# Kernel optimization log

Measured on AMD Instinct MI355X. Metric: run time of the kernel, lower is better.

## Reference

```python
import jax, jax.numpy as jnp
import numpy as np

# --- static mask-construction config (mirrors FlexAttnFunc.init_mask args) ---
B = 1
L_F, L_H, L_W = 8, 20, 36      # latent_shape[2:]
A_F, A_H, A_W = 8, 1, 1        # action_shape[2:]
PATCH = (1, 2, 2)
CHUNK = 1
PAD = 176
WINDOW = 6
DIM, HEADS, DHEAD = 1536, 12, 128
EPS = 1e-5


def _make_ids():
    lf, lh, lw = L_F // PATCH[0], L_H // PATCH[1], L_W // PATCH[2]
    lat_seq = np.repeat(np.arange(B), lf * lh * lw)
    act_seq = np.repeat(np.arange(B), A_F * A_H * A_W)
    seq = np.concatenate([lat_seq, lat_seq, act_seq, act_seq])
    lat_fr = np.broadcast_to(np.arange(L_F)[None, :, None, None], (B, L_F, lh, lw)).reshape(-1)
    act_fr = np.broadcast_to(np.arange(A_F)[None, :, None, None], (B, A_F, A_H, A_W)).reshape(-1)
    fr = np.concatenate([lat_fr // CHUNK * 2] * 2 + [act_fr // CHUNK * 2 + 1] * 2)
    nz = np.concatenate([np.zeros_like(lat_fr), np.ones_like(lat_fr),
                         np.zeros_like(act_fr), np.ones_like(act_fr)])
    pad = np.full(PAD, -1, dtype=np.int64)
    return (np.concatenate([seq, pad]).astype(np.int32),
            np.concatenate([fr, pad]).astype(np.int32),
            np.concatenate([nz, pad]).astype(np.int32))


def setup_inputs() -> dict:
    key = jax.random.key(0)
    ks = jax.random.split(key, 8)
    seq, fr, nz = _make_ids()
    S = seq.shape[0]  # 3072
    sd = 0.02
    return {
        'x': jax.random.normal(ks[0], (1, S, DIM), jnp.float32),
        'Wq': jax.random.normal(ks[1], (DIM, DIM), jnp.float32) * sd,
        'bq': jnp.zeros((DIM,), jnp.float32),
        'Wk': jax.random.normal(ks[2], (DIM, DIM), jnp.float32) * sd,
        'bk': jnp.zeros((DIM,), jnp.float32),
        'Wv': jax.random.normal(ks[3], (DIM, DIM), jnp.float32) * sd,
        'bv': jnp.zeros((DIM,), jnp.float32),
        'gq': 1.0 + jax.random.normal(ks[4], (DIM,), jnp.float32) * sd,
        'gk': 1.0 + jax.random.normal(ks[5], (DIM,), jnp.float32) * sd,
        'Wo': jax.random.normal(ks[6], (DIM, DIM), jnp.float32) * sd,
        'bo': jnp.zeros((DIM,), jnp.float32),
        'seq_ids': jnp.asarray(seq),
        'frame_ids': jnp.asarray(fr),
        'noise_ids': jnp.asarray(nz),
        'window_size': WINDOW,
    }


def _rms(u, g):
    # torch.nn.RMSNorm over last dim (size heads*dim_head), elementwise affine
    return u * jax.lax.rsqrt(jnp.mean(u * u, axis=-1, keepdims=True) + EPS) * g


def _mask(seq_ids, frame_ids, noise_ids, window_size):
    sq, sk = seq_ids[:, None], seq_ids[None, :]
    fq, fk = frame_ids[:, None], frame_ids[None, :]
    nq, nk = noise_ids[:, None], noise_ids[None, :]
    seq_ok = (sq == sk) & (sq >= 0) & (sk >= 0)
    c2c = (nq == 1) & (nk == 1) & (fk <= fq)      # clean->clean, block causal incl self
    n2c = (nq == 0) & (nk == 1) & (fk < fq)       # noise->clean, causal excl self
    n2n = (nq == 0) & (nk == 0) & (fk == fq)      # noise->noise, same frame only
    win = jnp.abs(fq - fk) <= window_size
    return (c2c | n2c | n2n) & seq_ok & win


def reference(x, Wq, bq, Wk, bk, Wv, bv, gq, gk, Wo, bo,
              seq_ids, frame_ids, noise_ids, window_size):
    S = x.shape[1]
    q = _rms(x @ Wq + bq, gq)[0].reshape(S, HEADS, DHEAD)
    k = _rms(x @ Wk + bk, gk)[0].reshape(S, HEADS, DHEAD)
    v = (x @ Wv + bv)[0].reshape(S, HEADS, DHEAD)
    mask = _mask(seq_ids, frame_ids, noise_ids, window_size)  # [S,S] bool
    scores = jnp.einsum('qhd,khd->hqk', q, k) * (DHEAD ** -0.5)
    scores = jnp.where(mask[None], scores, jnp.float32(-1e9))
    attn = jax.nn.softmax(scores, axis=-1)
    o = jnp.einsum('hqk,khd->qhd', attn, v)
    # zero out padded (fully-masked) query rows
    o = o * (seq_ids >= 0).astype(o.dtype)[:, None, None]
    y = o.reshape(1, S, HEADS * DHEAD) @ Wo + bo
    return y
```

## Files before the change

### kernel.cpp

```cpp
#include <hip/hip_runtime.h>
#include <hip/hip_bf16.h>
#include <stdint.h>

typedef __bf16 bf16x8 __attribute__((ext_vector_type(8)));
typedef float f32x4 __attribute__((ext_vector_type(4)));

__device__ __forceinline__ unsigned short f2bf(float f) {
  union { float f; unsigned int u; } v; v.f = f;
  unsigned int u = v.u;
  unsigned int r = (u + 0x7fffu + ((u >> 16) & 1u)) >> 16;
  return (unsigned short)r;
}

__global__ __launch_bounds__(256) void conv_f2bf(const float* __restrict__ in,
                                                 unsigned short* __restrict__ out, int n4) {
  int i = blockIdx.x * 256 + threadIdx.x;
  if (i < n4) {
    float4 v = ((const float4*)in)[i];
    ushort4 o;
    o.x = f2bf(v.x); o.y = f2bf(v.y); o.z = f2bf(v.z); o.w = f2bf(v.w);
    ((ushort4*)out)[i] = o;
  }
}

__global__ __launch_bounds__(256) void prep_bitmap(const int* __restrict__ seq,
                                                   const int* __restrict__ fr,
                                                   const int* __restrict__ nz,
                                                   const int* __restrict__ wsz,
                                                   unsigned long long* __restrict__ tbm,
                                                   int S) {
  __shared__ int ks_[3072];
  __shared__ unsigned int tm_[96];
  int tid = threadIdx.x, W = wsz[0];
  for (int i = tid; i < S; i += 256) {
    int sq = seq[i];
    ks_[i] = (sq < 0) ? 0 : ((1 << 9) | ((nz[i] & 1) << 8) | (fr[i] & 15) | (sq << 10));
  }
  __syncthreads();
  for (int t = tid; t < S / 32; t += 256) {
    unsigned int m = 0;
    for (int j = 0; j < 32; j++) {
      int a = ks_[t * 32 + j];
      if (a & (1 << 9)) m |= (a & (1 << 8)) ? (1u << (16 + (a & 15))) : (1u << (a & 15));
    }
    tm_[t] = m;
  }
  __syncthreads();
  for (int qg = tid; qg < S / 16; qg += 256) {
    unsigned int allowed = 0;
    for (int j = 0; j < 16; j++) {
      int a = ks_[qg * 16 + j];
      if (!(a & (1 << 9))) continue;
      int fq = a & 15, nq = (a >> 8) & 1;
      int lo = fq - W; if (lo < 0) lo = 0;
      unsigned int lom = ~((1u << lo) - 1);
      if (nq) allowed |= (((1u << (fq + 1)) - 1) & lom) << 16;
      else    allowed |= ((((1u << fq) - 1) & lom) << 16) | (1u << fq);
    }
    unsigned long long b0 = 0, b1 = 0;
    for (int t = 0; t < 96; t++)
      if (tm_[t] & allowed) { if (t < 64) b0 |= 1ull << t; else b1 |= 1ull << (t - 64); }
    tbm[qg * 2] = b0; tbm[qg * 2 + 1] = b1;
  }
}

__global__ __launch_bounds__(256) void prep_mask(const int* __restrict__ seq,
                                                 const int* __restrict__ fr,
                                                 const int* __restrict__ nz,
                                                 const int* __restrict__ wsz,
                                                 unsigned char* __restrict__ mb, int S) {
  int qg = blockIdx.y, t0 = blockIdx.x * 4;
  __shared__ int qs[16], qf_[16], qn[16], ksq[128], kfr[128], knz[128];
  int tid = threadIdx.x;
  if (tid < 16) {
    int q = qg * 16 + tid; qs[tid] = seq[q]; qf_[tid] = fr[q]; qn[tid] = nz[q];
  } else if (tid < 144) {
    int i = tid - 16; int k = t0 * 32 + i;
    ksq[i] = seq[k]; kfr[i] = fr[k]; knz[i] = nz[k];
  }
  __syncthreads();
  int wave = tid >> 6, lane = tid & 63, quad = lane >> 4, l16 = lane & 15;
  int W = wsz[0];
  unsigned int byte = 0;
  for (int nt = 0; nt < 2; nt++)
    for (int r = 0; r < 4; r++) {
      int qi = quad * 4 + r;
      int ki = wave * 32 + nt * 16 + l16;
      bool ok  = (qs[qi] == ksq[ki]) && (qs[qi] >= 0) && (ksq[ki] >= 0);
      bool c2c = (qn[qi] == 1) && (knz[ki] == 1) && (kfr[ki] <= qf_[qi]);
      bool n2c = (qn[qi] == 0) && (knz[ki] == 1) && (kfr[ki] <  qf_[qi]);
      bool n2n = (qn[qi] == 0) && (knz[ki] == 0) && (kfr[ki] == qf_[qi]);
      int df = qf_[qi] - kfr[ki]; df = df < 0 ? -df : df;
      if ((c2c || n2c || n2n) && ok && (df <= W)) byte |= 1u << (nt * 4 + r);
    }
  mb[((size_t)qg * 96 + t0 + wave) * 64 + lane] = (unsigned char)byte;
}

__global__ __launch_bounds__(256) void conv_wt4(const float* __restrict__ W0,
                                                const float* __restrict__ W1,
                                                const float* __restrict__ W2,
                                                const float* __restrict__ W3,
                                                unsigned short* __restrict__ Wt) {
  const int K = 1536, N = 1536;
  const float* W = blockIdx.z == 0 ? W0 : (blockIdx.z == 1 ? W1 : (blockIdx.z == 2 ? W2 : W3));
  __shared__ __align__(16) unsigned short t[64][65];
  int k0 = blockIdx.x * 64, n0 = blockIdx.y * 64;
  for (int i = 0; i < 16; i++) {
    int e = threadIdx.x + i * 256;
    int r = e >> 6, c = e & 63;
    t[r][c] = f2bf(W[(size_t)(k0 + r) * N + n0 + c]);
  }
  __syncthreads();
  for (int i = 0; i < 16; i++) {
    int e = threadIdx.x + i * 256;
    int r = e >> 6, c = e & 63;
    Wt[(size_t)(blockIdx.z * 1536 + n0 + r) * K + k0 + c] = t[c][r];
  }
}

__global__ __launch_bounds__(256) void gemm_qkv(
    const unsigned short* __restrict__ A, const unsigned short* __restrict__ Bt,
    const float* __restrict__ bq, const float* __restrict__ bk, const float* __restrict__ bv,
    float* __restrict__ linq, float* __restrict__ link, unsigned short* __restrict__ vtb,
    int S) {
  const int K = 1536;
  __shared__ __align__(16) unsigned short As[128 * 64];
  __shared__ __align__(16) unsigned short Bs[128 * 64];
  int tid = threadIdx.x, wave = tid >> 6, lane = tid & 63;
  int quad = lane >> 4, l16 = lane & 15;
  int m0 = blockIdx.x * 128, n0 = blockIdx.y * 128;
  int wm = (wave & 1) * 64, wn = (wave >> 1) * 64;
  int lr = lane >> 3, lc = (lane & 7) * 8;
  f32x4 acc[4][4] = {};
  for (int k0 = 0; k0 < K; k0 += 64) {
    for (int c = 0; c < 4; c++) {
      int chunk = wave * 4 + c;
      int row = chunk * 8 + lr;
      const unsigned short* ga = &A[(size_t)(m0 + row) * K + k0 + lc];
      const unsigned short* gb = &Bt[(size_t)(n0 + row) * K + k0 + lc];
      __builtin_amdgcn_global_load_lds(
          (const __attribute__((address_space(1))) unsigned int*)ga,
          (__attribute__((address_space(3))) unsigned int*)(As + chunk * 512), 16, 0, 0);
      __builtin_amdgcn_global_load_lds(
          (const __attribute__((address_space(1))) unsigned int*)gb,
          (__attribute__((address_space(3))) unsigned int*)(Bs + chunk * 512), 16, 0, 0);
    }
    __syncthreads();
    for (int kk = 0; kk < 64; kk += 32) {
      bf16x8 af[4], bfr[4];
      for (int i = 0; i < 4; i++)
        af[i] = *(const bf16x8*)&As[(wm + i * 16 + l16) * 64 + kk + quad * 8];
      for (int j = 0; j < 4; j++)
        bfr[j] = *(const bf16x8*)&Bs[(wn + j * 16 + l16) * 64 + kk + quad * 8];
      for (int i = 0; i < 4; i++)
        for (int j = 0; j < 4; j++)
          acc[i][j] = __builtin_amdgcn_mfma_f32_16x16x32_bf16(af[i], bfr[j], acc[i][j], 0, 0, 0);
    }
    __syncthreads();
  }
  int region = (n0 >= 3072) ? 2 : (n0 >= 1536 ? 1 : 0);
  int cbase = n0 - region * 1536;
  if (region < 2) {
    float* lin = region == 0 ? linq : link;
    const float* bias = region == 0 ? bq : bk;
    for (int j = 0; j < 4; j++) {
      int col = cbase + wn + j * 16 + l16;
      float b = bias[col];
      for (int i = 0; i < 4; i++)
        for (int r = 0; r < 4; r++)
          lin[(size_t)(m0 + wm + i * 16 + quad * 4 + r) * 1536 + col] = acc[i][j][r] + b;
    }
  } else {
    for (int j = 0; j < 4; j++) {
      int d = cbase + wn + j * 16 + l16;
      float b = bv[d];
      int hh = d >> 7, dd = d & 127;
      for (int i = 0; i < 4; i++)
        for (int r = 0; r < 4; r++) {
          int s = m0 + wm + i * 16 + quad * 4 + r;
          vtb[((size_t)(hh * 96 + (s >> 5)) * 128 + dd) * 32 + (s & 31)] = f2bf(acc[i][j][r] + b);
        }
    }
  }
}

__global__ __launch_bounds__(256) void gemm_wo(
    const unsigned short* __restrict__ A, const unsigned short* __restrict__ Bt,
    const float* __restrict__ bias, float* __restrict__ C, int M, int N, int K) {
  __shared__ __align__(16) unsigned short As[128 * 64];
  __shared__ __align__(16) unsigned short Bs[64 * 64];
  int tid = threadIdx.x, wave = tid >> 6, lane = tid & 63;
  int quad = lane >> 4, l16 = lane & 15;
  int m0 = blockIdx.x * 128, n0 = blockIdx.y * 64;
  int wm = (wave & 1) * 64, wn = (wave >> 1) * 32;
  int lr = lane >> 3, lc = (lane & 7) * 8;
  f32x4 acc[4][2] = {};
  for (int k0 = 0; k0 < K; k0 += 64) {
    for (int c = 0; c < 4; c++) {
      int chunk = wave * 4 + c;
      int row = chunk * 8 + lr;
      const unsigned short* ga = &A[(size_t)(m0 + row) * K + k0 + lc];
      __builtin_amdgcn_global_load_lds(
          (const __attribute__((address_space(1))) unsigned int*)ga,
          (__attribute__((address_space(3))) unsigned int*)(As + chunk * 512), 16, 0, 0);
    }
    for (int c = 0; c < 2; c++) {
      int chunk = wave * 2 + c;
      int row = chunk * 8 + lr;
      const unsigned short* gb = &Bt[(size_t)(n0 + row) * K + k0 + lc];
      __builtin_amdgcn_global_load_lds(
          (const __attribute__((address_space(1))) unsigned int*)gb,
          (__attribute__((address_space(3))) unsigned int*)(Bs + chunk * 512), 16, 0, 0);
    }
    __syncthreads();
    for (int kk = 0; kk < 64; kk += 32) {
      bf16x8 af[4], bfr[2];
      for (int i = 0; i < 4; i++)
        af[i] = *(const bf16x8*)&As[(wm + i * 16 + l16) * 64 + kk + quad * 8];
      for (int j = 0; j < 2; j++)
        bfr[j] = *(const bf16x8*)&Bs[(wn + j * 16 + l16) * 64 + kk + quad * 8];
      for (int i = 0; i < 4; i++)
        for (int j = 0; j < 2; j++)
          acc[i][j] = __builtin_amdgcn_mfma_f32_16x16x32_bf16(af[i], bfr[j], acc[i][j], 0, 0, 0);
    }
    __syncthreads();
  }
  for (int j = 0; j < 2; j++) {
    int col = n0 + wn + j * 16 + l16;
    float b = bias[col];
    for (int i = 0; i < 4; i++)
      for (int r = 0; r < 4; r++)
        C[(size_t)(m0 + wm + i * 16 + quad * 4 + r) * N + col] = acc[i][j][r] + b;
  }
}

__global__ __launch_bounds__(256) void rms_bf16(const float* __restrict__ lin,
                                                const float* __restrict__ g,
                                                unsigned short* __restrict__ out,
                                                int mode) {
  const int N = 1536;
  int row = blockIdx.x;
  const float* p = lin + (size_t)row * N;
  float vals[6];
  float ss = 0.f;
  for (int j = 0; j < 6; j++) {
    float v = p[threadIdx.x + j * 256];
    vals[j] = v; ss += v * v;
  }
  for (int o = 32; o > 0; o >>= 1) ss += __shfl_down(ss, o);
  __shared__ float red[4];
  if ((threadIdx.x & 63) == 0) red[threadIdx.x >> 6] = ss;
  __syncthreads();
  float tot = red[0] + red[1] + red[2] + red[3];
  float sc = rsqrtf(tot * (1.0f / N) + 1e-5f);
  for (int j = 0; j < 6; j++) {
    int c = threadIdx.x + j * 256;
    int hh = c >> 7, dd = c & 127;
    unsigned short v = f2bf(vals[j] * sc * g[c]);
    if (mode == 1)
      out[(((size_t)(hh * 96 + (row >> 5)) * 32) + (row & 31)) * 128 + dd] = v;
    else
      out[(((size_t)(hh * 192 + (row >> 4)) * 16) + (row & 15)) * 128 + dd] = v;
  }
}

__global__ __launch_bounds__(256) void attn(
    const unsigned short* __restrict__ qt,
    const unsigned short* __restrict__ kt,
    const unsigned short* __restrict__ vt,
    const unsigned char* __restrict__ mb,
    const unsigned long long* __restrict__ tbm,
    float* __restrict__ op0, float* __restrict__ op1,
    float* __restrict__ lp, int S) {
  const int h = blockIdx.x;
  const int qb64 = blockIdx.y;
  const int split = blockIdx.z;
  int tid = threadIdx.x, wave = tid >> 6, lane = tid & 63;
  int quad = lane >> 4, l16 = lane & 15;
  const float scale = 0.088388347648318447f;

  __shared__ __align__(16) unsigned short Ks[2][4096];
  __shared__ __align__(16) unsigned short Vs[2][4096];
  __shared__ __align__(16) unsigned short pshare[4][16][40];

  int qg = qb64 * 4 + wave;
  unsigned long long bm0 = tbm[(qb64 * 4) * 2]     | tbm[(qb64 * 4 + 1) * 2] |
                           tbm[(qb64 * 4 + 2) * 2] | tbm[(qb64 * 4 + 3) * 2];
  unsigned long long bm1 = tbm[(qb64 * 4) * 2 + 1]     | tbm[(qb64 * 4 + 1) * 2 + 1] |
                           tbm[(qb64 * 4 + 2) * 2 + 1] | tbm[(qb64 * 4 + 3) * 2 + 1];
  unsigned long long wb0 = tbm[qg * 2], wb1 = tbm[qg * 2 + 1];

  const unsigned short* kth = kt + (size_t)h * 96 * 4096;
  const unsigned short* vth = vt + (size_t)h * 96 * 4096;
  const unsigned char* mbq = mb + (size_t)qg * 96 * 64;

  bf16x8 qf[4];
  {
    const unsigned short* qp = qt + ((size_t)(h * 192 + qg) * 16 + l16) * 128 + quad * 8;
    for (int ks = 0; ks < 4; ks++) qf[ks] = *(const bf16x8*)&qp[ks * 32];
  }

  f32x4 oacc[8] = {};
  f32x4 lacc = {};
  const __bf16 onebf = (__bf16)1.0f;
  const bf16x8 ones = {onebf, onebf, onebf, onebf, onebf, onebf, onebf, onebf};

#define POP(dst) do { \
    if (bm0) { dst = __builtin_ctzll(bm0); bm0 &= bm0 - 1; } \
    else if (bm1) { dst = 64 + __builtin_ctzll(bm1); bm1 &= bm1 - 1; } \
    else dst = -1; } while (0)

#define STAGE(t_, b_) do { \
    for (int j = 0; j < 2; j++) { \
      int slot = j * 256 + tid; \
      int key = slot >> 4, cc = slot & 15; \
      const unsigned short* src = kth + (size_t)(t_) * 4096 + key * 128 + (cc ^ (key & 15)) * 8; \
      __builtin_amdgcn_global_load_lds( \
          (const __attribute__((address_space(1))) unsigned int*)src, \
          (__attribute__((address_space(3))) unsigned int*)(&Ks[b_][0] + j * 2048 + wave * 512), \
          16, 0, 0); \
    } \
    for (int j = 0; j < 2; j++) { \
      int slot = j * 256 + tid; \
      int row = slot >> 2, cc = slot & 3; \
      const unsigned short* src = vth + (size_t)(t_) * 4096 + row * 32 + (cc ^ ((row >> 1) & 3)) * 8; \
      __builtin_amdgcn_global_load_lds( \
          (const __attribute__((address_space(1))) unsigned int*)src, \
          (__attribute__((address_space(3))) unsigned int*)(&Vs[b_][0] + j * 2048 + wave * 512), \
          16, 0, 0); \
    } } while (0)

  int t, dsc;
  if (split) POP(dsc);
  POP(t);
  unsigned int mbyte = 0;
  if (t >= 0) { STAGE(t, 0); mbyte = mbq[t * 64 + lane]; }
  __syncthreads();
  int buf = 0;

  while (t >= 0) {
    POP(dsc);
    int tn; POP(tn);
    unsigned int mbyte2 = 0;
    if (tn >= 0) { STAGE(tn, buf ^ 1); mbyte2 = mbq[tn * 64 + lane]; }

    bool live = (t < 64) ? ((wb0 >> t) & 1) : ((wb1 >> (t - 64)) & 1);
    if (live) {
      f32x4 sacc[2] = {};
      for (int nt = 0; nt < 2; nt++) {
        int key = nt * 16 + l16;
        for (int ks = 0; ks < 4; ks++) {
          int cc = (ks * 4 + quad) ^ l16;
          bf16x8 kf = *(const bf16x8*)&Ks[buf][(key * 16 + cc) * 8];
          sacc[nt] = __builtin_amdgcn_mfma_f32_16x16x32_bf16(qf[ks], kf, sacc[nt], 0, 0, 0);
        }
      }
      for (int nt = 0; nt < 2; nt++)
        for (int r = 0; r < 4; r++) {
          float e = __expf(sacc[nt][r] * scale - 16.0f);
          float p = ((mbyte >> (nt * 4 + r)) & 1) ? e : 0.0f;
          pshare[wave][quad * 4 + r][nt * 16 + l16] = f2bf(p);
        }
      __asm__ __volatile__("s_waitcnt lgkmcnt(0)" ::: "memory");
      bf16x8 pf = *(const bf16x8*)&pshare[wave][l16][quad * 8];
      for (int d = 0; d < 8; d++) {
        int row = d * 16 + l16;
        int cc = quad ^ ((l16 >> 1) & 3);
        bf16x8 vf = *(const bf16x8*)&Vs[buf][(row * 4 + cc) * 8];
        oacc[d] = __builtin_amdgcn_mfma_f32_16x16x32_bf16(pf, vf, oacc[d], 0, 0, 0);
      }
      lacc = __builtin_amdgcn_mfma_f32_16x16x32_bf16(pf, ones, lacc, 0, 0, 0);
    }
    __syncthreads();
    buf ^= 1;
    t = tn;
    mbyte = mbyte2;
  }
#undef POP
#undef STAGE

  float* po = split ? op1 : op0;
  for (int r = 0; r < 4; r++) {
    int q = qb64 * 64 + wave * 16 + quad * 4 + r;
    for (int d = 0; d < 8; d++)
      po[((size_t)h * S + q) * 128 + d * 16 + l16] = oacc[d][r];
    if (l16 == 0)
      lp[((size_t)split * 12 + h) * S + q] = lacc[r];
  }
}

__global__ __launch_bounds__(256) void combine(const float* __restrict__ op0,
                                               const float* __restrict__ op1,
                                               const float* __restrict__ lp,
                                               const int* __restrict__ seq,
                                               unsigned short* __restrict__ ob, int S) {
  int e4 = blockIdx.x * 256 + threadIdx.x;
  int idx = e4 * 4;
  int per_h = S * 128;
  int h = idx / per_h;
  int rem = idx - h * per_h;
  int q = rem >> 7, dd = rem & 127;
  float l = lp[(size_t)h * S + q] + lp[(size_t)(12 + h) * S + q];
  float inv = (seq[q] >= 0 && l > 0.f) ? 1.0f / l : 0.0f;
  float4 a = ((const float4*)op0)[e4];
  float4 b = ((const float4*)op1)[e4];
  ushort4 o;
  o.x = f2bf((a.x + b.x) * inv);
  o.y = f2bf((a.y + b.y) * inv);
  o.z = f2bf((a.z + b.z) * inv);
  o.w = f2bf((a.w + b.w) * inv);
  *(ushort4*)&ob[(size_t)q * 1536 + h * 128 + dd] = o;
}

extern "C" void kernel_launch(void* const* d_in, const int* in_sizes, int n_in,
                              void* d_out, int out_size, void* d_ws, size_t ws_size,
                              hipStream_t stream) {
  const float* x  = (const float*)d_in[0];
  const float* Wq = (const float*)d_in[1];
  const float* bq = (const float*)d_in[2];
  const float* Wk = (const float*)d_in[3];
  const float* bk = (const float*)d_in[4];
  const float* Wv = (const float*)d_in[5];
  const float* bv = (const float*)d_in[6];
  const float* gq = (const float*)d_in[7];
  const float* gk = (const float*)d_in[8];
  const float* Wo = (const float*)d_in[9];
  const float* bo = (const float*)d_in[10];
  const int* seq  = (const int*)d_in[11];
  const int* fr   = (const int*)d_in[12];
  const int* nz   = (const int*)d_in[13];
  const int* wsz  = (const int*)d_in[14];
  float* out = (float*)d_out;
  const int S = in_sizes[11];
  const int D = 1536;

  char* ws = (char*)d_ws;
  size_t off = 0;
  unsigned short* x_bf = (unsigned short*)(ws + off); off += (size_t)S * D * 2;
  unsigned short* wt   = (unsigned short*)(ws + off); off += (size_t)4 * D * D * 2;
  float*          linq = (float*)(ws + off);          off += (size_t)S * D * 4;
  float*          link = (float*)(ws + off);          off += (size_t)S * D * 4;
  unsigned short* qt   = (unsigned short*)(ws + off); off += (size_t)S * D * 2;
  unsigned short* kt   = (unsigned short*)(ws + off); off += (size_t)S * D * 2;
  unsigned short* vtb  = (unsigned short*)(ws + off); off += (size_t)S * D * 2;
  unsigned short* o_bf = (unsigned short*)(ws + off); off += (size_t)S * D * 2;
  unsigned long long* tbm = (unsigned long long*)(ws + off); off += (size_t)(S / 16) * 16;
  unsigned char*  mbuf = (unsigned char*)(ws + off);  off += (size_t)(S / 16) * 96 * 64;
  float*          lp   = (float*)(ws + off);          off += (size_t)2 * 12 * S * 4;

  dim3 blk(256);
  conv_f2bf<<<dim3((S * D / 4 + 255) / 256), blk, 0, stream>>>(x, x_bf, S * D / 4);
  prep_bitmap<<<dim3(1), blk, 0, stream>>>(seq, fr, nz, wsz, tbm, S);
  prep_mask<<<dim3(24, S / 16), blk, 0, stream>>>(seq, fr, nz, wsz, mbuf, S);
  conv_wt4<<<dim3(D / 64, D / 64, 4), blk, 0, stream>>>(Wq, Wk, Wv, Wo, wt);
  gemm_qkv<<<dim3(S / 128, 3 * D / 128), blk, 0, stream>>>(x_bf, wt, bq, bk, bv,
                                                           linq, link, vtb, S);
  rms_bf16<<<dim3(S), blk, 0, stream>>>(linq, gq, qt, 2);
  rms_bf16<<<dim3(S), blk, 0, stream>>>(link, gk, kt, 1);
  attn<<<dim3(D / 128, S / 64, 2), blk, 0, stream>>>(qt, kt, vtb, mbuf, tbm,
                                                     linq, link, lp, S);
  combine<<<dim3(12 * S * 128 / 4 / 256), blk, 0, stream>>>(linq, link, lp, seq, o_bf, S);
  gemm_wo<<<dim3(S / 128, D / 64), blk, 0, stream>>>(o_bf, wt + (size_t)3 * D * D,
                                                     bo, out, S, D, D);
}
```

Measured before the change: 329.3 us.

## Fuse RMS sum-of-squares into QKV GEMM epilogue and store bf16 partial outputs

The QKV GEMM epilogue now writes Q and K directly as bf16 in the attention layouts and accumulates per-row sums of squares into a global buffer with atomics. A small rms_scale kernel then rescales the bf16 values in place, replacing the fp32 linear intermediates and the two rms_bf16 passes. Attention split partials are normalized and stored as bf16 instead of fp32, and combine reweights them by their row sums. This is meant to cut fp32 intermediate traffic, at the cost of an extra bf16 rounding before normalization, atomic contention, and a memset launch.

```diff
diff --git a/kernel.cpp b/kernel.cpp
--- a/kernel.cpp
+++ b/kernel.cpp
@@ -10,6 +10,9 @@
   unsigned int u = v.u;
   unsigned int r = (u + 0x7fffu + ((u >> 16) & 1u)) >> 16;
   return (unsigned short)r;
+}
+__device__ __forceinline__ float bf2f(unsigned short s) {
+  union { unsigned int u; float f; } v; v.u = ((unsigned int)s) << 16; return v.f;
 }
 
 __global__ __launch_bounds__(256) void conv_f2bf(const float* __restrict__ in,
@@ -121,8 +124,8 @@
 __global__ __launch_bounds__(256) void gemm_qkv(
     const unsigned short* __restrict__ A, const unsigned short* __restrict__ Bt,
     const float* __restrict__ bq, const float* __restrict__ bk, const float* __restrict__ bv,
-    float* __restrict__ linq, float* __restrict__ link, unsigned short* __restrict__ vtb,
-    int S) {
+    unsigned short* __restrict__ qt, unsigned short* __restrict__ ktb,
+    unsigned short* __restrict__ vtb, float* __restrict__ ssq, int S) {
   const int K = 1536;
   __shared__ __align__(16) unsigned short As[128 * 64];
   __shared__ __align__(16) unsigned short Bs[128 * 64];
@@ -161,15 +164,32 @@
   int region = (n0 >= 3072) ? 2 : (n0 >= 1536 ? 1 : 0);
   int cbase = n0 - region * 1536;
   if (region < 2) {
-    float* lin = region == 0 ? linq : link;
     const float* bias = region == 0 ? bq : bk;
+    unsigned short* outp = region == 0 ? qt : ktb;
+    float* ssqp = ssq + region * 3072;
+    float ss[4][4] = {};
     for (int j = 0; j < 4; j++) {
       int col = cbase + wn + j * 16 + l16;
       float b = bias[col];
-      for (int i = 0; i < 4; i++)
-        for (int r = 0; r < 4; r++)
-          lin[(size_t)(m0 + wm + i * 16 + quad * 4 + r) * 1536 + col] = acc[i][j][r] + b;
-    }
+      int hh = col >> 7, dd = col & 127;
+      for (int i = 0; i < 4; i++)
+        for (int r = 0; r < 4; r++) {
+          float v = acc[i][j][r] + b;
+          ss[i][r] += v * v;
+          int s = m0 + wm + i * 16 + quad * 4 + r;
+          size_t idx = (region == 0)
+            ? (((size_t)(hh * 192 + (s >> 4)) * 16 + (s & 15)) * 128 + dd)
+            : (((size_t)(hh * 96  + (s >> 5)) * 32 + (s & 31)) * 128 + dd);
+          outp[idx] = f2bf(v);
+        }
+    }
+    for (int i = 0; i < 4; i++)
+      for (int r = 0; r < 4; r++) {
+        float v = ss[i][r];
+        for (int o = 1; o < 16; o <<= 1) v += __shfl_xor(v, o);
+        if (l16 == 0)
+          atomicAdd(&ssqp[m0 + wm + i * 16 + quad * 4 + r], v);
+      }
   } else {
     for (int j = 0; j < 4; j++) {
       int d = cbase + wn + j * 16 + l16;
@@ -182,6 +202,32 @@
         }
     }
   }
+}
+
+__global__ __launch_bounds__(192) void rms_scale(unsigned short* __restrict__ qt,
+                                                 unsigned short* __restrict__ ktb,
+                                                 const float* __restrict__ ssq,
+                                                 const float* __restrict__ gq,
+                                                 const float* __restrict__ gk) {
+  int row = blockIdx.x, buf = blockIdx.y;
+  unsigned short* p = buf ? ktb : qt;
+  const float* g = buf ? gk : gq;
+  float sc = rsqrtf(ssq[buf * 3072 + row] * (1.0f / 1536.0f) + 1e-5f);
+  int c = threadIdx.x * 8;
+  int hh = c >> 7, dd = c & 127;
+  size_t idx = buf
+    ? (((size_t)(hh * 96  + (row >> 5)) * 32 + (row & 31)) * 128 + dd)
+    : (((size_t)(hh * 192 + (row >> 4)) * 16 + (row & 15)) * 128 + dd);
+  ushort4 a = *(ushort4*)&p[idx];
+  ushort4 b = *(ushort4*)&p[idx + 4];
+  float4 g0 = *(const float4*)&g[c];
+  float4 g1 = *(const float4*)&g[c + 4];
+  a.x = f2bf(bf2f(a.x) * sc * g0.x); a.y = f2bf(bf2f(a.y) * sc * g0.y);
+  a.z = f2bf(bf2f(a.z) * sc * g0.z); a.w = f2bf(bf2f(a.w) * sc * g0.w);
+  b.x = f2bf(bf2f(b.x) * sc * g1.x); b.y = f2bf(bf2f(b.y) * sc * g1.y);
+  b.z = f2bf(bf2f(b.z) * sc * g1.z); b.w = f2bf(bf2f(b.w) * sc * g1.w);
+  *(ushort4*)&p[idx] = a;
+  *(ushort4*)&p[idx + 4] = b;
 }
 
 __global__ __launch_bounds__(256) void gemm_wo(
@@ -234,43 +280,13 @@
   }
 }
 
-__global__ __launch_bounds__(256) void rms_bf16(const float* __restrict__ lin,
-                                                const float* __restrict__ g,
-                                                unsigned short* __restrict__ out,
-                                                int mode) {
-  const int N = 1536;
-  int row = blockIdx.x;
-  const float* p = lin + (size_t)row * N;
-  float vals[6];
-  float ss = 0.f;
-  for (int j = 0; j < 6; j++) {
-    float v = p[threadIdx.x + j * 256];
-    vals[j] = v; ss += v * v;
-  }
-  for (int o = 32; o > 0; o >>= 1) ss += __shfl_down(ss, o);
-  __shared__ float red[4];
-  if ((threadIdx.x & 63) == 0) red[threadIdx.x >> 6] = ss;
-  __syncthreads();
-  float tot = red[0] + red[1] + red[2] + red[3];
-  float sc = rsqrtf(tot * (1.0f / N) + 1e-5f);
-  for (int j = 0; j < 6; j++) {
-    int c = threadIdx.x + j * 256;
-    int hh = c >> 7, dd = c & 127;
-    unsigned short v = f2bf(vals[j] * sc * g[c]);
-    if (mode == 1)
-      out[(((size_t)(hh * 96 + (row >> 5)) * 32) + (row & 31)) * 128 + dd] = v;
-    else
-      out[(((size_t)(hh * 192 + (row >> 4)) * 16) + (row & 15)) * 128 + dd] = v;
-  }
-}
-
 __global__ __launch_bounds__(256) void attn(
     const unsigned short* __restrict__ qt,
     const unsigned short* __restrict__ kt,
     const unsigned short* __restrict__ vt,
     const unsigned char* __restrict__ mb,
     const unsigned long long* __restrict__ tbm,
-    float* __restrict__ op0, float* __restrict__ op1,
+    unsigned short* __restrict__ op0b, unsigned short* __restrict__ op1b,
     float* __restrict__ lp, int S) {
   const int h = blockIdx.x;
   const int qb64 = blockIdx.y;
@@ -379,18 +395,19 @@
 #undef POP
 #undef STAGE
 
-  float* po = split ? op1 : op0;
+  unsigned short* po = split ? op1b : op0b;
   for (int r = 0; r < 4; r++) {
     int q = qb64 * 64 + wave * 16 + quad * 4 + r;
+    float inv = (lacc[r] > 0.f) ? 1.0f / lacc[r] : 0.0f;
     for (int d = 0; d < 8; d++)
-      po[((size_t)h * S + q) * 128 + d * 16 + l16] = oacc[d][r];
+      po[((size_t)h * S + q) * 128 + d * 16 + l16] = f2bf(oacc[d][r] * inv);
     if (l16 == 0)
       lp[((size_t)split * 12 + h) * S + q] = lacc[r];
   }
 }
 
-__global__ __launch_bounds__(256) void combine(const float* __restrict__ op0,
-                                               const float* __restrict__ op1,
+__global__ __launch_bounds__(256) void combine(const unsigned short* __restrict__ op0b,
+                                               const unsigned short* __restrict__ op1b,
                                                const float* __restrict__ lp,
                                                const int* __restrict__ seq,
                                                unsigned short* __restrict__ ob, int S) {
@@ -400,15 +417,17 @@
   int h = idx / per_h;
   int rem = idx - h * per_h;
   int q = rem >> 7, dd = rem & 127;
-  float l = lp[(size_t)h * S + q] + lp[(size_t)(12 + h) * S + q];
-  float inv = (seq[q] >= 0 && l > 0.f) ? 1.0f / l : 0.0f;
-  float4 a = ((const float4*)op0)[e4];
-  float4 b = ((const float4*)op1)[e4];
+  float l0 = lp[(size_t)h * S + q], l1 = lp[(size_t)(12 + h) * S + q];
+  float tot = l0 + l1;
+  float ok = (seq[q] >= 0 && tot > 0.f) ? 1.0f / tot : 0.0f;
+  float w0 = l0 * ok, w1 = l1 * ok;
+  ushort4 a = ((const ushort4*)op0b)[e4];
+  ushort4 b = ((const ushort4*)op1b)[e4];
   ushort4 o;
-  o.x = f2bf((a.x + b.x) * inv);
-  o.y = f2bf((a.y + b.y) * inv);
-  o.z = f2bf((a.z + b.z) * inv);
-  o.w = f2bf((a.w + b.w) * inv);
+  o.x = f2bf(bf2f(a.x) * w0 + bf2f(b.x) * w1);
+  o.y = f2bf(bf2f(a.y) * w0 + bf2f(b.y) * w1);
+  o.z = f2bf(bf2f(a.z) * w0 + bf2f(b.z) * w1);
+  o.w = f2bf(bf2f(a.w) * w0 + bf2f(b.w) * w1);
   *(ushort4*)&ob[(size_t)q * 1536 + h * 128 + dd] = o;
 }
 
@@ -438,28 +457,29 @@
   size_t off = 0;
   unsigned short* x_bf = (unsigned short*)(ws + off); off += (size_t)S * D * 2;
   unsigned short* wt   = (unsigned short*)(ws + off); off += (size_t)4 * D * D * 2;
-  float*          linq = (float*)(ws + off);          off += (size_t)S * D * 4;
-  float*          link = (float*)(ws + off);          off += (size_t)S * D * 4;
   unsigned short* qt   = (unsigned short*)(ws + off); off += (size_t)S * D * 2;
-  unsigned short* kt   = (unsigned short*)(ws + off); off += (size_t)S * D * 2;
+  unsigned short* ktb  = (unsigned short*)(ws + off); off += (size_t)S * D * 2;
   unsigned short* vtb  = (unsigned short*)(ws + off); off += (size_t)S * D * 2;
   unsigned short* o_bf = (unsigned short*)(ws + off); off += (size_t)S * D * 2;
+  unsigned short* op0b = (unsigned short*)(ws + off); off += (size_t)S * D * 2;
+  unsigned short* op1b = (unsigned short*)(ws + off); off += (size_t)S * D * 2;
   unsigned long long* tbm = (unsigned long long*)(ws + off); off += (size_t)(S / 16) * 16;
   unsigned char*  mbuf = (unsigned char*)(ws + off);  off += (size_t)(S / 16) * 96 * 64;
   float*          lp   = (float*)(ws + off);          off += (size_t)2 * 12 * S * 4;
+  float*          ssq  = (float*)(ws + off);          off += (size_t)2 * 3072 * 4;
 
   dim3 blk(256);
   conv_f2bf<<<dim3((S * D / 4 + 255) / 256), blk, 0, stream>>>(x, x_bf, S * D / 4);
   prep_bitmap<<<dim3(1), blk, 0, stream>>>(seq, fr, nz, wsz, tbm, S);
   prep_mask<<<dim3(24, S / 16), blk, 0, stream>>>(seq, fr, nz, wsz, mbuf, S);
   conv_wt4<<<dim3(D / 64, D / 64, 4), blk, 0, stream>>>(Wq, Wk, Wv, Wo, wt);
+  hipMemsetAsync(ssq, 0, (size_t)2 * 3072 * 4, stream);
   gemm_qkv<<<dim3(S / 128, 3 * D / 128), blk, 0, stream>>>(x_bf, wt, bq, bk, bv,
-                                                           linq, link, vtb, S);
-  rms_bf16<<<dim3(S), blk, 0, stream>>>(linq, gq, qt, 2);
-  rms_bf16<<<dim3(S), blk, 0, stream>>>(link, gk, kt, 1);
-  attn<<<dim3(D / 128, S / 64, 2), blk, 0, stream>>>(qt, kt, vtb, mbuf, tbm,
-                                                     linq, link, lp, S);
-  combine<<<dim3(12 * S * 128 / 4 / 256), blk, 0, stream>>>(linq, link, lp, seq, o_bf, S);
+                                                           qt, ktb, vtb, ssq, S);
+  rms_scale<<<dim3(S, 2), dim3(192), 0, stream>>>(qt, ktb, ssq, gq, gk);
+  attn<<<dim3(D / 128, S / 64, 2), blk, 0, stream>>>(qt, ktb, vtb, mbuf, tbm,
+                                                     op0b, op1b, lp, S);
+  combine<<<dim3(12 * S * 128 / 4 / 256), blk, 0, stream>>>(op0b, op1b, lp, seq, o_bf, S);
   gemm_wo<<<dim3(S / 128, D / 64), blk, 0, stream>>>(o_bf, wt + (size_t)3 * D * D,
                                                      bo, out, S, D, D);
 }
```

After: 323.1 us. No clear change (-1.9%).
